# Kernel optimization log

Hardware: AMD Instinct MI355X
Metric: run time of the kernel (lower is better)

Reference implementation:

```python
import jax, jax.numpy as jnp
import numpy as np

D = 1024      # n_embedding
H = 16        # n_head
DH = D // H   # head_size = 64
T = 2048      # block_size / seq len
B = 2
EPS = 1e-5


def layer_norm(x, gamma, beta):
    mu = jnp.mean(x, axis=-1, keepdims=True)
    var = jnp.mean((x - mu) ** 2, axis=-1, keepdims=True)
    return (x - mu) * jax.lax.rsqrt(var + EPS) * gamma + beta


def setup_inputs() -> dict:
    key = jax.random.key(0)
    ks = jax.random.split(key, 12)
    s = 0.02
    return {
        "x": jax.random.normal(ks[0], (B, T, D), jnp.float32),
        # per-head QKV projections stacked over heads: [H, D, DH] (no bias, as in Head)
        "wq": jax.random.normal(ks[1], (H, D, DH), jnp.float32) * s,
        "wk": jax.random.normal(ks[2], (H, D, DH), jnp.float32) * s,
        "wv": jax.random.normal(ks[3], (H, D, DH), jnp.float32) * s,
        # output projection [H*DH, D] with bias
        "w_proj": jax.random.normal(ks[4], (H * DH, D), jnp.float32) * s,
        "b_proj": jnp.zeros((D,), jnp.float32),
        # feedforward: D -> 4D -> D
        "w1": jax.random.normal(ks[5], (D, 4 * D), jnp.float32) * s,
        "b1": jnp.zeros((4 * D,), jnp.float32),
        "w2": jax.random.normal(ks[6], (4 * D, D), jnp.float32) * s,
        "b2": jnp.zeros((D,), jnp.float32),
        # layer norms
        "ln1_g": jnp.ones((D,), jnp.float32),
        "ln1_b": jnp.zeros((D,), jnp.float32),
        "ln2_g": jnp.ones((D,), jnp.float32),
        "ln2_b": jnp.zeros((D,), jnp.float32),
    }


def reference(x, wq, wk, wv, w_proj, b_proj, w1, b1, w2, b2,
              ln1_g, ln1_b, ln2_g, ln2_b):
    # pre-LN attention sub-block
    xn = layer_norm(x, ln1_g, ln1_b)                      # [B,T,D]
    q = jnp.einsum('btd,hdk->bhtk', xn, wq)               # [B,H,T,DH]
    k = jnp.einsum('btd,hdk->bhtk', xn, wk)
    v = jnp.einsum('btd,hdk->bhtk', xn, wv)
    scale = DH ** -0.5
    scores = jnp.einsum('bhtk,bhsk->bhts', q, k) * scale  # [B,H,T,T]
    causal = jnp.tril(jnp.ones((T, T), bool))
    scores = jnp.where(causal, scores, -jnp.inf)
    attn = jax.nn.softmax(scores, axis=-1)
    out = jnp.einsum('bhts,bhsk->bhtk', attn, v)          # [B,H,T,DH]
    out = out.transpose(0, 2, 1, 3).reshape(B, T, H * DH)  # concat heads
    x = x + out @ w_proj + b_proj                          # residual 1
    # pre-LN feedforward sub-block
    xn2 = layer_norm(x, ln2_g, ln2_b)
    h = jax.nn.relu(xn2 @ w1 + b1)
    x = x + h @ w2 + b2                                    # residual 2
    return x
```

## Files before the change

### kernel.cpp

```cpp
#include <hip/hip_runtime.h>
#include <hip/hip_bf16.h>
#include <math.h>


#define D_MODEL 1024
#define NH 16
#define DHEAD 64
#define SEQ 2048
#define NTOK 4096

typedef __bf16 bf16x8 __attribute__((ext_vector_type(8)));
typedef float f32x4 __attribute__((ext_vector_type(4)));
typedef float f32x16 __attribute__((ext_vector_type(16)));
typedef unsigned short u16x8 __attribute__((ext_vector_type(8)));

__device__ __forceinline__ unsigned short f2b(float f) {
  unsigned u = __builtin_bit_cast(unsigned, f);
  u = u + 0x7fffu + ((u >> 16) & 1u);
  return (unsigned short)(u >> 16);
}

__device__ __forceinline__ bf16x8 ld_bf16x8(const unsigned short* p) {
  u16x8 u = *(const u16x8*)p;
  return __builtin_bit_cast(bf16x8, u);
}

__device__ __forceinline__ void async16(void* lds, const void* g) {
  __builtin_amdgcn_global_load_lds(
      (const __attribute__((address_space(1))) unsigned int*)g,
      (__attribute__((address_space(3))) unsigned int*)lds, 16, 0, 0);
}

__device__ __forceinline__ bf16x8 ds_read16(const void* p) {
  bf16x8 r;
  unsigned a = (unsigned)(size_t)(const __attribute__((address_space(3))) void*)p;
  asm volatile("ds_read_b128 %0, %1" : "=v"(r) : "v"(a));
  return r;
}
__device__ __forceinline__ void ds_write32(void* p, unsigned v) {
  unsigned a = (unsigned)(size_t)(__attribute__((address_space(3))) void*)p;
  asm volatile("ds_write_b32 %0, %1" :: "v"(a), "v"(v));
}
__device__ __forceinline__ unsigned cvt_pk_bf16(float lo, float hi) {
  unsigned d;
  asm("v_cvt_pk_bf16_f32 %0, %1, %2" : "=v"(d) : "v"(lo), "v"(hi));
  return d;
}
#define WAIT_LGKM0_FENCE() do { \
  asm volatile("s_waitcnt lgkmcnt(0)" ::: "memory"); \
  __builtin_amdgcn_sched_barrier(0); } while (0)


__global__ __launch_bounds__(256) void repack_qkv(
    const float* __restrict__ wq, const float* __restrict__ wk,
    const float* __restrict__ wv, unsigned short* __restrict__ outT) {
  __shared__ float tile[64][65];
  int t = blockIdx.x;
  int sel = t >> 8;
  int h = (t >> 4) & 15;
  int rt = t & 15;
  const float* in = (sel == 0 ? wq : sel == 1 ? wk : wv) + (size_t)h * D_MODEL * DHEAD;
  int d0 = rt * 64;
  for (int i = 0; i < 16; i++) {
    int idx = i * 256 + threadIdx.x;
    int r = idx >> 6, c = idx & 63;
    tile[r][c] = in[(size_t)(d0 + r) * DHEAD + c];
  }
  __syncthreads();
  unsigned short* ob = outT + (size_t)(sel * 1024 + h * 64) * D_MODEL + d0;
  for (int i = 0; i < 16; i++) {
    int idx = i * 256 + threadIdx.x;
    int c = idx >> 6, r = idx & 63;
    ob[(size_t)c * D_MODEL + r] = f2b(tile[r][c]);
  }
}

__global__ __launch_bounds__(256) void transpose_to_bf16(
    const float* __restrict__ in, unsigned short* __restrict__ out, int R, int C) {
  __shared__ float tile[64][65];
  int r0 = blockIdx.x * 64, c0 = blockIdx.y * 64;
  for (int i = 0; i < 16; i++) {
    int idx = i * 256 + threadIdx.x;
    int r = idx >> 6, c = idx & 63;
    tile[r][c] = in[(size_t)(r0 + r) * C + c0 + c];
  }
  __syncthreads();
  for (int i = 0; i < 16; i++) {
    int idx = i * 256 + threadIdx.x;
    int c = idx >> 6, r = idx & 63;
    out[(size_t)(c0 + c) * R + r0 + r] = f2b(tile[r][c]);
  }
}

__global__ __launch_bounds__(256) void layernorm_bf16(
    const float* __restrict__ x, const float* __restrict__ g,
    const float* __restrict__ bta, unsigned short* __restrict__ out) {
  int row = blockIdx.x;
  int tid = threadIdx.x;
  const float4* xr = (const float4*)(x + (size_t)row * D_MODEL);
  float4 v = xr[tid];
  float s = v.x + v.y + v.z + v.w;
  float s2 = v.x * v.x + v.y * v.y + v.z * v.z + v.w * v.w;
  for (int m = 1; m < 64; m <<= 1) {
    s += __shfl_xor(s, m);
    s2 += __shfl_xor(s2, m);
  }
  __shared__ float ps[4], ps2[4];
  int wid = tid >> 6;
  if ((tid & 63) == 0) { ps[wid] = s; ps2[wid] = s2; }
  __syncthreads();
  float S = ps[0] + ps[1] + ps[2] + ps[3];
  float S2 = ps2[0] + ps2[1] + ps2[2] + ps2[3];
  float mu = S * (1.f / D_MODEL);
  float var = S2 * (1.f / D_MODEL) - mu * mu;
  float inv = rsqrtf(var + 1e-5f);
  float4 gv = ((const float4*)g)[tid];
  float4 bv = ((const float4*)bta)[tid];
  ushort4 o;
  o.x = f2b((v.x - mu) * inv * gv.x + bv.x);
  o.y = f2b((v.y - mu) * inv * gv.y + bv.y);
  o.z = f2b((v.z - mu) * inv * gv.z + bv.z);
  o.w = f2b((v.w - mu) * inv * gv.w + bv.w);
  ((ushort4*)(out + (size_t)row * D_MODEL))[tid] = o;
}

template <int MODE>
__global__ __launch_bounds__(256, 2) void gemm_bt(
    const unsigned short* __restrict__ A, const unsigned short* __restrict__ BT,
    int M, int N, int K,
    const float* __restrict__ bias, const float* __restrict__ resid,
    float* __restrict__ outF, unsigned short* __restrict__ outB,
    unsigned short* __restrict__ outQ, unsigned short* __restrict__ outK,
    unsigned short* __restrict__ outV) {
  __shared__ alignas(16) unsigned short lsA[128 * 64];
  __shared__ alignas(16) unsigned short lsB[128 * 64];
  const int tid = threadIdx.x;
  const int wid = tid >> 6, lane = tid & 63;
  const int lr = lane & 15, lg = lane >> 4;
  const int row0 = blockIdx.x * 128, col0 = blockIdx.y * 128;
  const int wr = (wid >> 1) * 64, wc = (wid & 1) * 64;
  f32x4 acc[4][4] = {};
  const int nk = K >> 6;
  for (int kt = 0; kt < nk; ++kt) {
    const int k0 = kt << 6;
    if (kt) __syncthreads();
#pragma unroll
    for (int i = 0; i < 4; i++) {
      int sidx = i * 256 + tid;
      int r = sidx >> 3, s = sidx & 7;
      int ss = s ^ (r & 7);
      async16((char*)lsA + (i * 256 + wid * 64) * 16,
              A + (size_t)(row0 + r) * K + k0 + ss * 8);
      async16((char*)lsB + (i * 256 + wid * 64) * 16,
              BT + (size_t)(col0 + r) * K + k0 + ss * 8);
    }
    __syncthreads();
#pragma unroll
    for (int kk = 0; kk < 2; ++kk) {
      bf16x8 af[4], bfr[4];
#pragma unroll
      for (int m = 0; m < 4; m++) {
        int r = wr + m * 16 + lr;
        int sw = (kk * 4 + lg) ^ (r & 7);
        af[m] = *(const bf16x8*)((const char*)lsA + r * 128 + sw * 16);
      }
#pragma unroll
      for (int n = 0; n < 4; n++) {
        int r = wc + n * 16 + lr;
        int sw = (kk * 4 + lg) ^ (r & 7);
        bfr[n] = *(const bf16x8*)((const char*)lsB + r * 128 + sw * 16);
      }
#pragma unroll
      for (int m = 0; m < 4; m++)
#pragma unroll
        for (int n = 0; n < 4; n++)
          acc[m][n] = __builtin_amdgcn_mfma_f32_16x16x32_bf16(af[m], bfr[n], acc[m][n], 0, 0, 0);
    }
  }
#pragma unroll
  for (int m = 0; m < 4; m++) {
#pragma unroll
    for (int n = 0; n < 4; n++) {
#pragma unroll
      for (int r2 = 0; r2 < 4; r2++) {
        int row = row0 + wr + m * 16 + lg * 4 + r2;
        int col = col0 + wc + n * 16 + lr;
        float v = acc[m][n][r2];
        if constexpr (MODE == 0) {
          v += bias[col] + resid[(size_t)row * N + col];
          outF[(size_t)row * N + col] = v;
        } else if constexpr (MODE == 1) {
          v += bias[col];
          v = fmaxf(v, 0.f);
          outB[(size_t)row * N + col] = f2b(v);
        } else {
          int sel = col >> 10, jj = col & 1023, h = jj >> 6, dh = jj & 63;
          int b = row >> 11, t = row & 2047;
          size_t bh = (size_t)(b * NH + h);
          if (sel == 0)      outQ[(bh * SEQ + t) * DHEAD + dh] = f2b(v);
          else if (sel == 1) outK[(bh * SEQ + t) * DHEAD + dh] = f2b(v);
          else               outV[(bh * DHEAD + dh) * SEQ + t] = f2b(v);
        }
      }
    }
  }
}

template <int TAG>
__global__ __launch_bounds__(512, 1) void gemm_bt8(
    const unsigned short* __restrict__ A, const unsigned short* __restrict__ BT,
    int M, int N, int K,
    const float* __restrict__ bias, const float* __restrict__ resid,
    float* __restrict__ outF) {
  __shared__ alignas(16) unsigned short lsA[3][128 * 64];
  __shared__ alignas(16) unsigned short lsB[3][128 * 64];
  const int tid = threadIdx.x;
  const int wid = tid >> 6, lane = tid & 63;
  const int lr = lane & 15, lg = lane >> 4;
  const int row0 = blockIdx.x * 128, col0 = blockIdx.y * 128;
  const int wr = (wid >> 2) * 64, wc = (wid & 3) * 32;
  f32x4 acc[4][2] = {};
  const int nk = K >> 6;

  auto STAGE = [&](int bi, int kt) {
    const int k0 = kt << 6;
#pragma unroll
    for (int i = 0; i < 2; i++) {
      int sidx = i * 512 + tid;
      int r = sidx >> 3, s = sidx & 7;
      int ss = s ^ (r & 7);
      async16((char*)lsA[bi] + (i * 512 + wid * 64) * 16,
              A + (size_t)(row0 + r) * K + k0 + ss * 8);
      async16((char*)lsB[bi] + (i * 512 + wid * 64) * 16,
              BT + (size_t)(col0 + r) * K + k0 + ss * 8);
    }
  };

  STAGE(0, 0);
  if (nk > 1) STAGE(1, 1);
  for (int kt = 0; kt < nk; ++kt) {
    const int cur = kt % 3;
    if (kt + 2 < nk) {
      STAGE((kt + 2) % 3, kt + 2);
      asm volatile("s_waitcnt vmcnt(8)" ::: "memory");
    } else if (kt + 1 < nk) {
      asm volatile("s_waitcnt vmcnt(4)" ::: "memory");
    } else {
      asm volatile("s_waitcnt vmcnt(0)" ::: "memory");
    }
    __builtin_amdgcn_s_barrier();
    __builtin_amdgcn_sched_barrier(0);
#pragma unroll
    for (int kk = 0; kk < 2; ++kk) {
      bf16x8 af[4], bfr[2];
#pragma unroll
      for (int m = 0; m < 4; m++) {
        int r = wr + m * 16 + lr;
        int sw = (kk * 4 + lg) ^ (r & 7);
        af[m] = ds_read16((const char*)lsA[cur] + r * 128 + sw * 16);
      }
#pragma unroll
      for (int n = 0; n < 2; n++) {
        int r = wc + n * 16 + lr;
        int sw = (kk * 4 + lg) ^ (r & 7);
        bfr[n] = ds_read16((const char*)lsB[cur] + r * 128 + sw * 16);
      }
      WAIT_LGKM0_FENCE();
      __builtin_amdgcn_s_setprio(1);
#pragma unroll
      for (int m = 0; m < 4; m++)
#pragma unroll
        for (int n = 0; n < 2; n++)
          acc[m][n] = __builtin_amdgcn_mfma_f32_16x16x32_bf16(af[m], bfr[n], acc[m][n], 0, 0, 0);
      __builtin_amdgcn_s_setprio(0);
    }
    __builtin_amdgcn_sched_barrier(0);
    __builtin_amdgcn_s_barrier();
  }
#pragma unroll
  for (int m = 0; m < 4; m++) {
#pragma unroll
    for (int n = 0; n < 2; n++) {
#pragma unroll
      for (int r2 = 0; r2 < 4; r2++) {
        int row = row0 + wr + m * 16 + lg * 4 + r2;
        int col = col0 + wc + n * 16 + lr;
        float v = acc[m][n][r2] + bias[col] + resid[(size_t)row * N + col];
        outF[(size_t)row * N + col] = v;
      }
    }
  }
}

__global__ __launch_bounds__(512, 2) void gemm256_bt(
    const unsigned short* __restrict__ A, const unsigned short* __restrict__ BT,
    int M, int N, int K, int ntn,
    const float* __restrict__ bias, unsigned short* __restrict__ outB) {
  __shared__ alignas(16) unsigned short ls[2][2][2][256 * 32];
  const int tid = threadIdx.x;
  const int wid = tid >> 6, lane = tid & 63;
  const int lr = lane & 15, lg = lane >> 4;
  const int nwg = gridDim.x;
  const int wg = (blockIdx.x & 7) * (nwg >> 3) + (blockIdx.x >> 3);
  const int row0 = (wg / ntn) * 256, col0 = (wg % ntn) * 256;
  const int mbase = (wid >> 2) * 128;
  const int nbase = (wid & 3) * 64;

  f32x4 acc[8][4] = {};

  auto STAGE = [&](int buf, int kh, int ab, int kt) {
    const unsigned short* src = ab ? (BT + (size_t)col0 * K) : (A + (size_t)row0 * K);
    const int kbase = kt * 64 + kh * 32;
    unsigned short* dst0 = &ls[buf][kh][ab][0];
#pragma unroll
    for (int c = 0; c < 2; c++) {
      int s = c * 512 + tid;
      int row = s >> 2, c2 = s & 3;
      int ss = c2 ^ ((row >> 1) & 3);
      async16(dst0 + (size_t)(c * 512 + wid * 64) * 8,
              src + (size_t)row * K + kbase + ss * 8);
    }
  };
  auto LDA = [&](bf16x8* a, int buf, int kk, int mh) {
#pragma unroll
    for (int i = 0; i < 4; i++) {
      int mrow = mbase + (mh * 4 + i) * 16 + lr;
      int ch = lg ^ ((mrow >> 1) & 3);
      a[i] = ds_read16(&ls[buf][kk][0][mrow * 32 + ch * 8]);
    }
  };
  auto LDB = [&](bf16x8* b, int buf, int kk) {
#pragma unroll
    for (int i = 0; i < 4; i++) {
      int brow = nbase + i * 16 + lr;
      int ch = lg ^ ((brow >> 1) & 3);
      b[i] = ds_read16(&ls[buf][kk][1][brow * 32 + ch * 8]);
    }
  };

  const int nk = K >> 6;
  STAGE(0, 0, 0, 0); STAGE(0, 0, 1, 0); STAGE(0, 1, 0, 0); STAGE(0, 1, 1, 0);
  asm volatile("s_waitcnt vmcnt(4)" ::: "memory");
  __builtin_amdgcn_s_barrier();

  for (int t = 0; t < nk; ++t) {
    const int cur = t & 1, nxt = cur ^ 1;
    const bool haveNext = (t + 1 < nk);
    bf16x8 a[4], b[4];
    LDA(a, cur, 0, 0); LDB(b, cur, 0);
    if (haveNext) STAGE(nxt, 0, 0, t + 1);
    __builtin_amdgcn_s_barrier();
    WAIT_LGKM0_FENCE();
    __builtin_amdgcn_s_setprio(1);
#pragma unroll
    for (int i = 0; i < 4; i++)
#pragma unroll
      for (int j = 0; j < 4; j++)
        acc[i][j] = __builtin_amdgcn_mfma_f32_16x16x32_bf16(a[i], b[j], acc[i][j], 0, 0, 0);
    __builtin_amdgcn_s_setprio(0);
    __builtin_amdgcn_s_barrier();
    LDA(a, cur, 0, 1);
    if (haveNext) {
      STAGE(nxt, 0, 1, t + 1);
      asm volatile("s_waitcnt vmcnt(4)" ::: "memory");
    } else {
      asm volatile("s_waitcnt vmcnt(0)" ::: "memory");
    }
    __builtin_amdgcn_s_barrier();
    WAIT_LGKM0_FENCE();
    __builtin_amdgcn_s_setprio(1);
#pragma unroll
    for (int i = 0; i < 4; i++)
#pragma unroll
      for (int j = 0; j < 4; j++)
        acc[4 + i][j] = __builtin_amdgcn_mfma_f32_16x16x32_bf16(a[i], b[j], acc[4 + i][j], 0, 0, 0);
    __builtin_amdgcn_s_setprio(0);
    __builtin_amdgcn_s_barrier();
    LDA(a, cur, 1, 0); LDB(b, cur, 1);
    if (haveNext) STAGE(nxt, 1, 0, t + 1);
    __builtin_amdgcn_s_barrier();
    WAIT_LGKM0_FENCE();
    __builtin_amdgcn_s_setprio(1);
#pragma unroll
    for (int i = 0; i < 4; i++)
#pragma unroll
      for (int j = 0; j < 4; j++)
        acc[i][j] = __builtin_amdgcn_mfma_f32_16x16x32_bf16(a[i], b[j], acc[i][j], 0, 0, 0);
    __builtin_amdgcn_s_setprio(0);
    __builtin_amdgcn_s_barrier();
    LDA(a, cur, 1, 1);
    if (haveNext) {
      STAGE(nxt, 1, 1, t + 1);
      asm volatile("s_waitcnt vmcnt(4)" ::: "memory");
    }
    __builtin_amdgcn_s_barrier();
    WAIT_LGKM0_FENCE();
    __builtin_amdgcn_s_setprio(1);
#pragma unroll
    for (int i = 0; i < 4; i++)
#pragma unroll
      for (int j = 0; j < 4; j++)
        acc[4 + i][j] = __builtin_amdgcn_mfma_f32_16x16x32_bf16(a[i], b[j], acc[4 + i][j], 0, 0, 0);
    __builtin_amdgcn_s_setprio(0);
    __builtin_amdgcn_s_barrier();
  }
#pragma unroll
  for (int mi = 0; mi < 8; mi++) {
#pragma unroll
    for (int ni = 0; ni < 4; ni++) {
#pragma unroll
      for (int r2 = 0; r2 < 4; r2++) {
        int row = row0 + mbase + mi * 16 + lg * 4 + r2;
        int col = col0 + nbase + ni * 16 + lr;
        float v = acc[mi][ni][r2] + bias[col];
        outB[(size_t)row * N + col] = f2b(fmaxf(v, 0.f));
      }
    }
  }
}

__global__ __launch_bounds__(256, 4) void attn_fwd(
    const unsigned short* __restrict__ Q, const unsigned short* __restrict__ K,
    const unsigned short* __restrict__ VT, unsigned short* __restrict__ O) {
  __shared__ alignas(16) unsigned short Kl[2][4096];
  __shared__ alignas(16) unsigned short Vl[2][4096];
  const int tid = threadIdx.x, wid = tid >> 6, lane = tid & 63;
  const int l31 = lane & 31, h = lane >> 5;
  const int sid = (int)(blockIdx.x & 7) * 64 + (int)(blockIdx.x >> 3);
  const int bh = sid >> 4, qt = 15 - (sid & 15);
  const unsigned short* Qb = Q + (size_t)bh * SEQ * DHEAD;
  const unsigned short* Kb = K + (size_t)bh * SEQ * DHEAD;
  const unsigned short* Vb = VT + (size_t)bh * DHEAD * SEQ;
  const int q0w = qt * 128 + wid * 32;
  bf16x8 qf[4];
#pragma unroll
  for (int dk = 0; dk < 4; dk++)
    qf[dk] = ld_bf16x8(Qb + (size_t)(q0w + l31) * DHEAD + dk * 16 + h * 8);
  f32x16 o0 = {}, o1 = {};
  float psum = 0.f;
  const float cs = 0.18033688011112042f;
  const int ntiles = qt * 2 + 2;

  auto STAGE = [&](unsigned short* Kd, unsigned short* Vd, int s0) {
#pragma unroll
    for (int c = 0; c < 2; c++) {
      int s = c * 256 + tid;
      int row = s >> 3, sl = s & 7;
      int ss = sl ^ (row & 7);
      async16((char*)Kd + (c * 256 + wid * 64) * 16,
              Kb + (size_t)(s0 + row) * DHEAD + ss * 8);
      async16((char*)Vd + (c * 256 + wid * 64) * 16,
              Vb + (size_t)row * SEQ + s0 + ss * 8);
    }
  };

  STAGE(Kl[0], Vl[0], 0);
  for (int t = 0; t < ntiles; ++t) {
    if (t + 1 < ntiles) {
      STAGE(Kl[(t + 1) & 1], Vl[(t + 1) & 1], (t + 1) * 64);
      asm volatile("s_waitcnt vmcnt(4)" ::: "memory");
    } else {
      asm volatile("s_waitcnt vmcnt(0)" ::: "memory");
    }
    __builtin_amdgcn_s_barrier();
    __builtin_amdgcn_sched_barrier(0);
    const unsigned short* Kc = Kl[t & 1];
    const unsigned short* Vc = Vl[t & 1];
    const int s0 = t * 64;
    if (s0 < q0w + 32) {
      const bool needMask = (s0 + 63 > q0w);
#pragma unroll
      for (int g = 0; g < 2; g++) {
        bf16x8 kf[4], vf[4];
        {
          int krow = 32 * g + l31;
          int kbase_sw = krow & 7;
#pragma unroll
          for (int dk = 0; dk < 4; dk++) {
            int ch = (2 * dk + h) ^ kbase_sw;
            kf[dk] = ds_read16((const char*)Kc + krow * 128 + ch * 16);
          }
#pragma unroll
          for (int dg = 0; dg < 2; dg++) {
            int vrow = 32 * dg + l31;
            int vsw = vrow & 7;
#pragma unroll
            for (int c = 0; c < 2; c++) {
              int kk = 2 * g + c;
              int ch = (2 * kk + h) ^ vsw;
              vf[dg * 2 + c] = ds_read16((const char*)Vc + vrow * 128 + ch * 16);
            }
          }
        }
        WAIT_LGKM0_FENCE();
        f32x16 st = {};
#pragma unroll
        for (int dk = 0; dk < 4; dk++)
          st = __builtin_amdgcn_mfma_f32_32x32x16_bf16(kf[dk], qf[dk], st, 0, 0, 0);
        float p[16];
#pragma unroll
        for (int reg = 0; reg < 16; reg++) {
          float xx = st[reg] * cs;
          if (needMask) {
            int kg = s0 + 32 * g + (reg & 3) + 8 * (reg >> 2) + 4 * h;
            if (kg > q0w + l31) xx = -INFINITY;
          }
          float e = __builtin_amdgcn_exp2f(xx);
          p[reg] = e;
          psum += e;
        }
        unsigned w[8];
#pragma unroll
        for (int s = 0; s < 4; s++) {
          w[s * 2 + 0] = cvt_pk_bf16(p[s * 4 + 0], p[s * 4 + 1]);
          w[s * 2 + 1] = cvt_pk_bf16(p[s * 4 + 2], p[s * 4 + 3]);
        }
#pragma unroll
        for (int c = 0; c < 2; c++) {
          unsigned a0 = w[(2 * c) * 2 + 0], b0 = w[(2 * c + 1) * 2 + 0];
          unsigned a1 = w[(2 * c) * 2 + 1], b1 = w[(2 * c + 1) * 2 + 1];
          asm volatile("v_permlane32_swap_b32 %0, %1" : "+v"(a0), "+v"(b0));
          asm volatile("v_permlane32_swap_b32 %0, %1" : "+v"(a1), "+v"(b1));
          uint4 pw = {a0, a1, b0, b1};
          bf16x8 pf = __builtin_bit_cast(bf16x8, pw);
          o0 = __builtin_amdgcn_mfma_f32_32x32x16_bf16(vf[0 * 2 + c], pf, o0, 0, 0, 0);
          o1 = __builtin_amdgcn_mfma_f32_32x32x16_bf16(vf[1 * 2 + c], pf, o1, 0, 0, 0);
        }
      }
    }
    __builtin_amdgcn_sched_barrier(0);
    __builtin_amdgcn_s_barrier();
  }
  psum += __shfl_xor(psum, 32);
  float inv = 1.f / psum;
  unsigned short* slice = (unsigned short*)Kl + wid * 2048;
#pragma unroll
  for (int dg = 0; dg < 2; dg++) {
#pragma unroll
    for (int s = 0; s < 4; s++) {
#pragma unroll
      for (int m = 0; m < 2; m++) {
        float va = (dg ? o1[s * 4 + 2 * m] : o0[s * 4 + 2 * m]) * inv;
        float vb = (dg ? o1[s * 4 + 2 * m + 1] : o0[s * 4 + 2 * m + 1]) * inv;
        unsigned wv = cvt_pk_bf16(va, vb);
        int d = 32 * dg + 8 * s + 4 * h + 2 * m;
        ds_write32(&slice[l31 * 64 + d], wv);
      }
    }
  }
  WAIT_LGKM0_FENCE();
  bf16x8 ov[4];
#pragma unroll
  for (int pss = 0; pss < 4; pss++) {
    int qrow = pss * 8 + (lane >> 3);
    int d0 = (lane & 7) * 8;
    ov[pss] = ds_read16(&slice[qrow * 64 + d0]);
  }
  WAIT_LGKM0_FENCE();
  const int b = bh >> 4, head = bh & 15;
#pragma unroll
  for (int pss = 0; pss < 4; pss++) {
    int qrow = pss * 8 + (lane >> 3);
    int d0 = (lane & 7) * 8;
    *(bf16x8*)(O + ((size_t)b * SEQ + q0w + qrow) * D_MODEL + head * DHEAD + d0) = ov[pss];
  }
}


extern "C" void kernel_launch(void* const* d_in, const int* in_sizes, int n_in,
                              void* d_out, int out_size, void* d_ws, size_t ws_size,
                              hipStream_t stream) {
  const float* x = (const float*)d_in[0];
  const float* wq = (const float*)d_in[1];
  const float* wk = (const float*)d_in[2];
  const float* wv = (const float*)d_in[3];
  const float* w_proj = (const float*)d_in[4];
  const float* b_proj = (const float*)d_in[5];
  const float* w1 = (const float*)d_in[6];
  const float* b1 = (const float*)d_in[7];
  const float* w2 = (const float*)d_in[8];
  const float* b2 = (const float*)d_in[9];
  const float* ln1g = (const float*)d_in[10];
  const float* ln1b = (const float*)d_in[11];
  const float* ln2g = (const float*)d_in[12];
  const float* ln2b = (const float*)d_in[13];

  char* ws = (char*)d_ws;
  const size_t MB = 1024ull * 1024ull;
  unsigned short* xn = (unsigned short*)(ws + 0);
  unsigned short* Qb = (unsigned short*)(ws + 8 * MB);
  unsigned short* Kb = (unsigned short*)(ws + 16 * MB);
  unsigned short* VTb = (unsigned short*)(ws + 24 * MB);
  unsigned short* aout = (unsigned short*)(ws + 32 * MB);
  unsigned short* hbuf = (unsigned short*)(ws + 40 * MB);
  unsigned short* WqkvT = (unsigned short*)(ws + 72 * MB);
  unsigned short* wprojT = (unsigned short*)(ws + 78 * MB);
  unsigned short* w1T = (unsigned short*)(ws + 80 * MB);
  unsigned short* w2T = (unsigned short*)(ws + 88 * MB);
  float* x1 = (float*)d_out;

  repack_qkv<<<dim3(768), 256, 0, stream>>>(wq, wk, wv, WqkvT);
  transpose_to_bf16<<<dim3(16, 16), 256, 0, stream>>>(w_proj, wprojT, 1024, 1024);
  transpose_to_bf16<<<dim3(16, 64), 256, 0, stream>>>(w1, w1T, 1024, 4096);
  transpose_to_bf16<<<dim3(64, 16), 256, 0, stream>>>(w2, w2T, 4096, 1024);

  layernorm_bf16<<<NTOK, 256, 0, stream>>>(x, ln1g, ln1b, xn);
  gemm_bt<2><<<dim3(32, 24), 256, 0, stream>>>(xn, WqkvT, NTOK, 3072, 1024,
      nullptr, nullptr, nullptr, nullptr, Qb, Kb, VTb);
  attn_fwd<<<dim3(512), 256, 0, stream>>>(Qb, Kb, VTb, aout);
  gemm_bt8<0><<<dim3(32, 8), 512, 0, stream>>>(aout, wprojT, NTOK, 1024, 1024,
      b_proj, x, x1);
  layernorm_bf16<<<NTOK, 256, 0, stream>>>(x1, ln2g, ln2b, xn);
  gemm256_bt<<<dim3(256), 512, 0, stream>>>(xn, w1T, NTOK, 4096, 1024, 16,
      b1, hbuf);
  gemm_bt8<1><<<dim3(32, 8), 512, 0, stream>>>(hbuf, w2T, NTOK, 1024, 4096,
      b2, x1, (float*)d_out);
}
```

Baseline: 232.3 us.

## Double-buffer LDS in QKV GEMM to overlap global loads with MFMA

Converts the QKV projection GEMM from a single LDS buffer to a two-stage ping-pong buffer. The next K-tile is prefetched asynchronously while the current one is consumed, with explicit vmcnt waits and raw barriers replacing the full syncthreads. MFMA sections are also wrapped in s_setprio. Doubling LDS use to 64KB per block may limit occupancy to two blocks per CU, and it drops the unused MODE 1 path.

```diff
diff --git a/kernel.cpp b/kernel.cpp
--- a/kernel.cpp
+++ b/kernel.cpp
@@ -125,15 +125,15 @@
 }
 
 template <int MODE>
-__global__ __launch_bounds__(256, 2) void gemm_bt(
+__global__ __launch_bounds__(256, 2) void gemm_p4(
     const unsigned short* __restrict__ A, const unsigned short* __restrict__ BT,
     int M, int N, int K,
     const float* __restrict__ bias, const float* __restrict__ resid,
-    float* __restrict__ outF, unsigned short* __restrict__ outB,
+    float* __restrict__ outF,
     unsigned short* __restrict__ outQ, unsigned short* __restrict__ outK,
     unsigned short* __restrict__ outV) {
-  __shared__ alignas(16) unsigned short lsA[128 * 64];
-  __shared__ alignas(16) unsigned short lsB[128 * 64];
+  __shared__ alignas(16) unsigned short lsA[2][128 * 64];
+  __shared__ alignas(16) unsigned short lsB[2][128 * 64];
   const int tid = threadIdx.x;
   const int wid = tid >> 6, lane = tid & 63;
   const int lr = lane & 15, lg = lane >> 4;
@@ -141,20 +141,32 @@
   const int wr = (wid >> 1) * 64, wc = (wid & 1) * 64;
   f32x4 acc[4][4] = {};
   const int nk = K >> 6;
-  for (int kt = 0; kt < nk; ++kt) {
+
+  auto STAGE = [&](int bi, int kt) {
     const int k0 = kt << 6;
-    if (kt) __syncthreads();
 #pragma unroll
     for (int i = 0; i < 4; i++) {
       int sidx = i * 256 + tid;
       int r = sidx >> 3, s = sidx & 7;
       int ss = s ^ (r & 7);
-      async16((char*)lsA + (i * 256 + wid * 64) * 16,
+      async16((char*)lsA[bi] + (i * 256 + wid * 64) * 16,
               A + (size_t)(row0 + r) * K + k0 + ss * 8);
-      async16((char*)lsB + (i * 256 + wid * 64) * 16,
+      async16((char*)lsB[bi] + (i * 256 + wid * 64) * 16,
               BT + (size_t)(col0 + r) * K + k0 + ss * 8);
     }
-    __syncthreads();
+  };
+
+  STAGE(0, 0);
+  for (int kt = 0; kt < nk; ++kt) {
+    const int cur = kt & 1;
+    if (kt + 1 < nk) {
+      STAGE(cur ^ 1, kt + 1);
+      asm volatile("s_waitcnt vmcnt(8)" ::: "memory");
+    } else {
+      asm volatile("s_waitcnt vmcnt(0)" ::: "memory");
+    }
+    __builtin_amdgcn_s_barrier();
+    __builtin_amdgcn_sched_barrier(0);
 #pragma unroll
     for (int kk = 0; kk < 2; ++kk) {
       bf16x8 af[4], bfr[4];
@@ -162,20 +174,25 @@
       for (int m = 0; m < 4; m++) {
         int r = wr + m * 16 + lr;
         int sw = (kk * 4 + lg) ^ (r & 7);
-        af[m] = *(const bf16x8*)((const char*)lsA + r * 128 + sw * 16);
+        af[m] = ds_read16((const char*)lsA[cur] + r * 128 + sw * 16);
       }
 #pragma unroll
       for (int n = 0; n < 4; n++) {
         int r = wc + n * 16 + lr;
         int sw = (kk * 4 + lg) ^ (r & 7);
-        bfr[n] = *(const bf16x8*)((const char*)lsB + r * 128 + sw * 16);
-      }
+        bfr[n] = ds_read16((const char*)lsB[cur] + r * 128 + sw * 16);
+      }
+      WAIT_LGKM0_FENCE();
+      __builtin_amdgcn_s_setprio(1);
 #pragma unroll
       for (int m = 0; m < 4; m++)
 #pragma unroll
         for (int n = 0; n < 4; n++)
           acc[m][n] = __builtin_amdgcn_mfma_f32_16x16x32_bf16(af[m], bfr[n], acc[m][n], 0, 0, 0);
-    }
+      __builtin_amdgcn_s_setprio(0);
+    }
+    __builtin_amdgcn_sched_barrier(0);
+    __builtin_amdgcn_s_barrier();
   }
 #pragma unroll
   for (int m = 0; m < 4; m++) {
@@ -189,10 +206,6 @@
         if constexpr (MODE == 0) {
           v += bias[col] + resid[(size_t)row * N + col];
           outF[(size_t)row * N + col] = v;
-        } else if constexpr (MODE == 1) {
-          v += bias[col];
-          v = fmaxf(v, 0.f);
-          outB[(size_t)row * N + col] = f2b(v);
         } else {
           int sel = col >> 10, jj = col & 1023, h = jj >> 6, dh = jj & 63;
           int b = row >> 11, t = row & 2047;
@@ -605,8 +618,8 @@
   transpose_to_bf16<<<dim3(64, 16), 256, 0, stream>>>(w2, w2T, 4096, 1024);
 
   layernorm_bf16<<<NTOK, 256, 0, stream>>>(x, ln1g, ln1b, xn);
-  gemm_bt<2><<<dim3(32, 24), 256, 0, stream>>>(xn, WqkvT, NTOK, 3072, 1024,
-      nullptr, nullptr, nullptr, nullptr, Qb, Kb, VTb);
+  gemm_p4<2><<<dim3(32, 24), 256, 0, stream>>>(xn, WqkvT, NTOK, 3072, 1024,
+      nullptr, nullptr, nullptr, Qb, Kb, VTb);
   attn_fwd<<<dim3(512), 256, 0, stream>>>(Qb, Kb, VTb, aout);
   gemm_bt8<0><<<dim3(32, 8), 512, 0, stream>>>(aout, wprojT, NTOK, 1024, 1024,
       b_proj, x, x1);
```

New measurement: 232.5 us. About the same (+0.1%).
